# Kernel tuning notes

Hardware: AMD Instinct MI355X
Metric: run time of the kernel (lower is better)

The kernel has to match this reference:

```python
import jax, jax.numpy as jnp
import numpy as np

N_NODES = 100000
NNZ = 3200000
DIM = 256
HOPS = 3


def setup_inputs() -> dict:
    key = jax.random.key(0)
    ks = jax.random.split(key, 8)
    m = jax.random.normal(ks[0], (N_NODES, DIM), dtype=jnp.float32)
    vals = jax.random.uniform(ks[1], (NNZ,), dtype=jnp.float32)
    scale = 1.0 / np.sqrt(DIM)
    Wn = jax.random.normal(ks[2], (HOPS, DIM, DIM), dtype=jnp.float32) * scale
    bn = jax.random.normal(ks[3], (HOPS, DIM), dtype=jnp.float32) * 0.01
    Ws = jax.random.normal(ks[4], (HOPS, DIM, DIM), dtype=jnp.float32) * scale
    bs = jax.random.normal(ks[5], (HOPS, DIM), dtype=jnp.float32) * 0.01
    rows = jax.random.randint(ks[6], (NNZ,), 0, N_NODES, dtype=jnp.int64)
    cols = jax.random.randint(ks[7], (NNZ,), 0, N_NODES, dtype=jnp.int64)
    return {"m": m, "vals": vals, "Wn": Wn, "bn": bn, "Ws": Ws, "bs": bs,
            "rows": rows, "cols": cols}


def reference(m, vals, Wn, bn, Ws, bs, rows, cols):
    # GraphMerge.forward (dropout is identity at eval / rate 0):
    # per hop: H_n = SpMM(A, H) @ Wn^T + bn ; H_s = H @ Ws^T + bs ;
    # H = H_n + H_s ; ELU except after last hop.
    N = m.shape[0]
    hop_num = Wn.shape[0]
    H = m
    for i in range(hop_num):
        # SpMM via edge-list gather + segment_sum (same math as CSR matmul)
        msg = H[cols] * vals[:, None]                     # [nnz, d]
        Hn = jax.ops.segment_sum(msg, rows, num_segments=N)  # [N, d]
        Hn = Hn @ Wn[i].T + bn[i]
        Hs = H @ Ws[i].T + bs[i]
        H = Hn + Hs
        if i != hop_num - 1:
            H = jax.nn.elu(H)
    return H
```

## Files before the change

kernel.cpp:

```cpp
#include <hip/hip_runtime.h>
#include <hip/hip_bf16.h>

typedef unsigned short ushort_t;
using bf16x8 = __attribute__((ext_vector_type(8))) __bf16;
using f32x4  = __attribute__((ext_vector_type(4))) float;

#define NDIM 256

__device__ __forceinline__ float bf2f(ushort_t u) {
    union { unsigned int i; float f; } x; x.i = ((unsigned int)u) << 16; return x.f;
}
__device__ __forceinline__ ushort_t f2bf(float f) {
    unsigned int u = __float_as_uint(f);
    unsigned int r = (u + 0x7FFFu + ((u >> 16) & 1u)) >> 16;
    return (ushort_t)r;
}
__device__ __forceinline__ float ldf(const void* p, int i, int isbf) {
    return isbf ? bf2f(((const ushort_t*)p)[i]) : ((const float*)p)[i];
}
__device__ __forceinline__ int get_idx(const void* arr, int i, int is64) {
    if (is64) return (int)((const long long*)arr)[i];
    return ((const int*)arr)[i];
}

__global__ void k_probe(const unsigned int* __restrict__ w, int* __restrict__ flag) {
    __shared__ int cnt_in;
    if (threadIdx.x == 0) cnt_in = 0;
    __syncthreads();
    int local = 0;
    for (int i = threadIdx.x; i < 4096; i += blockDim.x) {
        unsigned int e = (w[i] >> 7) & 0xFFu;
        if (e >= 110u && e <= 135u) local++;
    }
    atomicAdd(&cnt_in, local);
    __syncthreads();
    if (threadIdx.x == 0) *flag = (cnt_in >= 2048) ? 1 : 0;
}

__global__ void k_detect(const unsigned int* __restrict__ rows_w, int nnz, int* __restrict__ flag) {
    __shared__ int nz;
    if (threadIdx.x == 0) nz = 0;
    __syncthreads();
    int samples = min(nnz / 2, 4096);
    for (int i = threadIdx.x; i < samples; i += blockDim.x) {
        if (rows_w[2 * i + 1] != 0u) atomicAdd(&nz, 1);
    }
    __syncthreads();
    if (threadIdx.x == 0) *flag = (nz == 0) ? 1 : 0;
}

__global__ void k_cvt_m(const void* __restrict__ src, ushort_t* __restrict__ dst, int n,
                        const int* __restrict__ flag) {
    int i = blockIdx.x * blockDim.x + threadIdx.x;
    if (i >= n) return;
    int isbf = *flag;
    dst[i] = isbf ? ((const ushort_t*)src)[i] : f2bf(((const float*)src)[i]);
}

__global__ void k_bias(const void* __restrict__ bn, const void* __restrict__ bs,
                       float* __restrict__ bc, int n, const int* __restrict__ flag) {
    int i = blockIdx.x * blockDim.x + threadIdx.x;
    if (i >= n) return;
    int isbf = *flag;
    bc[i] = ldf(bn, i, isbf) + ldf(bs, i, isbf);
}

__global__ void k_wpack(const void* __restrict__ Wn, const void* __restrict__ Ws,
                        ushort_t* __restrict__ bpack, int total, const int* __restrict__ flag) {
    int t = blockIdx.x * blockDim.x + threadIdx.x;
    if (t >= total) return;
    int isbf  = *flag;
    int j     = t & 7;
    int lane  = (t >> 3) & 63;
    int ntile = (t >> 9) & 15;
    int kstep = (t >> 13) & 15;
    int hop   = t >> 17;
    int k = (kstep << 5) + ((lane >> 4) << 3) + j;
    int n = (ntile << 4) + (lane & 15);
    int kk = k & 255;
    float w = (k < 256) ? ldf(Wn, hop * 65536 + n * 256 + kk, isbf)
                        : ldf(Ws, hop * 65536 + n * 256 + kk, isbf);
    ushort_t hi = f2bf(w);
    float lo = w - bf2f(hi);
    int base = ((((hop << 4) + kstep) << 5) + (ntile << 1)) * 512 + (lane << 3) + j;
    bpack[base]       = hi;
    bpack[base + 512] = f2bf(lo);
}

__global__ void k_hist(const void* __restrict__ rows, int* __restrict__ cnt, int nnz,
                       const int* __restrict__ flag) {
    int is64 = *flag;
    int i = blockIdx.x * blockDim.x + threadIdx.x;
    if (i < nnz) atomicAdd(&cnt[get_idx(rows, i, is64)], 1);
}

__global__ void k_chunksum(const int* __restrict__ cnt, int* __restrict__ csum, int n) {
    __shared__ int s[256];
    int i = blockIdx.x * 256 + threadIdx.x;
    int v = (i < n) ? cnt[i] : 0;
    s[threadIdx.x] = v;
    __syncthreads();
    for (int off = 128; off > 0; off >>= 1) {
        if (threadIdx.x < off) s[threadIdx.x] += s[threadIdx.x + off];
        __syncthreads();
    }
    if (threadIdx.x == 0) csum[blockIdx.x] = s[0];
}

__global__ void k_scanchunks(const int* __restrict__ csum, int* __restrict__ coff, int nchunks) {
    __shared__ int a[512], b[512];
    int t = threadIdx.x;
    int v = (t < nchunks) ? csum[t] : 0;
    a[t] = v;
    __syncthreads();
    int* src = a; int* dst = b;
    for (int off = 1; off < 512; off <<= 1) {
        dst[t] = src[t] + ((t >= off) ? src[t - off] : 0);
        __syncthreads();
        int* tmp = src; src = dst; dst = tmp;
    }
    if (t < nchunks) coff[t] = src[t] - v;
}

__global__ void k_scanwrite(const int* __restrict__ cnt, const int* __restrict__ coff,
                            int* __restrict__ row_start, int* __restrict__ row_cur,
                            int n, int nnz) {
    __shared__ int a[256], b[256];
    int t = threadIdx.x;
    int i = blockIdx.x * 256 + t;
    int v = (i < n) ? cnt[i] : 0;
    a[t] = v;
    __syncthreads();
    int* src = a; int* dst = b;
    for (int off = 1; off < 256; off <<= 1) {
        dst[t] = src[t] + ((t >= off) ? src[t - off] : 0);
        __syncthreads();
        int* tmp = src; src = dst; dst = tmp;
    }
    int excl = src[t] - v + coff[blockIdx.x];
    if (i < n) { row_start[i] = excl; row_cur[i] = excl; }
    if (i == n) row_start[n] = nnz;
}

__global__ void k_scatter(const void* __restrict__ rows, const void* __restrict__ cols,
                          const void* __restrict__ vals, int* __restrict__ row_cur,
                          int2* __restrict__ edata, int nnz,
                          const int* __restrict__ iflag, const int* __restrict__ fflag) {
    int is64 = *iflag;
    int isbf = *fflag;
    int i = blockIdx.x * blockDim.x + threadIdx.x;
    if (i >= nnz) return;
    int r = get_idx(rows, i, is64);
    int c = get_idx(cols, i, is64);
    float v = ldf(vals, i, isbf);
    int p = atomicAdd(&row_cur[r], 1);
    edata[p] = make_int2(c, __float_as_int(v));
}

__global__ void k_spmm(const ushort_t* __restrict__ hb, const int* __restrict__ row_start,
                       const int2* __restrict__ edata, ushort_t* __restrict__ hn, int n) {
    int wid = (blockIdx.x * blockDim.x + threadIdx.x) >> 6;
    if (wid >= n) return;
    wid = __builtin_amdgcn_readfirstlane(wid);
    int lane = threadIdx.x & 63;
    int e0 = row_start[wid];
    int e1 = row_start[wid + 1];
    float a0 = 0.f, a1 = 0.f, a2 = 0.f, a3 = 0.f;
    int off = lane * 4;
    for (int e = e0; e < e1; ++e) {
        int2 ed = edata[e];
        float v = __int_as_float(ed.y);
        ushort4 h = *reinterpret_cast<const ushort4*>(hb + (((long)ed.x) << 8) + off);
        a0 += bf2f(h.x) * v;
        a1 += bf2f(h.y) * v;
        a2 += bf2f(h.z) * v;
        a3 += bf2f(h.w) * v;
    }
    ushort4 o;
    o.x = f2bf(a0); o.y = f2bf(a1); o.z = f2bf(a2); o.w = f2bf(a3);
    *reinterpret_cast<ushort4*>(hn + (((long)wid) << 8) + off) = o;
}

__device__ __forceinline__ void stage32k(const ushort_t* __restrict__ src, ushort_t* dstlds, int tid) {
    const char* s = (const char*)src;
    char* d = (char*)dstlds;
    #pragma unroll
    for (int i = 0; i < 8; ++i) {
        int off = i * 4096 + tid * 16;
        __builtin_amdgcn_global_load_lds(
            (const __attribute__((address_space(1))) unsigned int*)(s + off),
            (__attribute__((address_space(3))) unsigned int*)(d + off),
            16, 0, 0);
    }
}

__global__ __launch_bounds__(256, 2) void k_gemm_mfma(
        const ushort_t* __restrict__ hn, const ushort_t* __restrict__ hb,
        const ushort_t* __restrict__ bpack, const float* __restrict__ bc,
        void* __restrict__ dst, int applyElu, int writeF32, int nvalid) {
    __shared__ __align__(16) ushort_t lds[2][16384];
    int tid  = threadIdx.x;
    int wave = tid >> 6, lane = tid & 63;
    int wm = wave >> 1, wn = wave & 1;
    int rowbase = blockIdx.x * 128 + wm * 64;
    int lr = lane & 15;
    int lk = (lane >> 4) << 3;

    f32x4 acc[4][8];
    #pragma unroll
    for (int mf = 0; mf < 4; ++mf)
        #pragma unroll
        for (int nf = 0; nf < 8; ++nf) acc[mf][nf] = (f32x4){0.f, 0.f, 0.f, 0.f};

    stage32k(bpack, &lds[0][0], tid);
    int cur = 0;
    #pragma unroll 1
    for (int ks = 0; ks < 16; ++ks) {
        const ushort_t* asrc = (ks < 8) ? hn : hb;
        int kcol = ((ks & 7) << 5) + lk;
        bf16x8 af[4];
        #pragma unroll
        for (int mf = 0; mf < 4; ++mf) {
            long row = rowbase + mf * 16 + lr;
            af[mf] = *(const bf16x8*)(asrc + (row << 8) + kcol);
        }
        if (ks < 15) stage32k(bpack + (ks + 1) * 16384, &lds[cur ^ 1][0], tid);
        __syncthreads();
        const ushort_t* bb = &lds[cur][0];
        #pragma unroll
        for (int nf = 0; nf < 8; ++nf) {
            const ushort_t* fp = bb + ((((wn << 3) + nf) << 1) << 9) + (lane << 3);
            bf16x8 bhi = *(const bf16x8*)(fp);
            bf16x8 blo = *(const bf16x8*)(fp + 512);
            #pragma unroll
            for (int mf = 0; mf < 4; ++mf) {
                acc[mf][nf] = __builtin_amdgcn_mfma_f32_16x16x32_bf16(af[mf], bhi, acc[mf][nf], 0, 0, 0);
                acc[mf][nf] = __builtin_amdgcn_mfma_f32_16x16x32_bf16(af[mf], blo, acc[mf][nf], 0, 0, 0);
            }
        }
        __syncthreads();
        cur ^= 1;
    }

    int colb = wn << 7;
    float bcv[8];
    #pragma unroll
    for (int nf = 0; nf < 8; ++nf) bcv[nf] = bc[colb + (nf << 4) + lr];
    int rsub = (lane >> 4) << 2;
    #pragma unroll
    for (int mf = 0; mf < 4; ++mf) {
        #pragma unroll
        for (int r = 0; r < 4; ++r) {
            int row = rowbase + mf * 16 + rsub + r;
            if (row < nvalid) {
                #pragma unroll
                for (int nf = 0; nf < 8; ++nf) {
                    float v = acc[mf][nf][r] + bcv[nf];
                    if (applyElu) v = (v > 0.f) ? v : expm1f(v);
                    int col = colb + (nf << 4) + lr;
                    if (writeF32) ((float*)dst)[(((long)row) << 8) + col] = v;
                    else          ((ushort_t*)dst)[(((long)row) << 8) + col] = f2bf(v);
                }
            }
        }
    }
}

extern "C" void kernel_launch(void* const* d_in, const int* in_sizes, int n_in,
                              void* d_out, int out_size, void* d_ws, size_t ws_size,
                              hipStream_t stream) {
    const void* m    = d_in[0];
    const void* vals = d_in[1];
    const void* Wn   = d_in[2];
    const void* bn   = d_in[3];
    const void* Ws   = d_in[4];
    const void* bs   = d_in[5];
    const void* rows = d_in[6];
    const void* cols = d_in[7];

    const int N    = in_sizes[0] / NDIM;
    const int nnz  = in_sizes[1];
    const int hops = in_sizes[3] / NDIM;
    const size_t mpad = ((size_t)N + 127) & ~(size_t)127;

    char* p = (char*)d_ws;
    ushort_t* Hb    = (ushort_t*)p; p += mpad * NDIM * 2;
    ushort_t* Hn    = (ushort_t*)p; p += mpad * NDIM * 2;
    ushort_t* Bpack = (ushort_t*)p; p += (size_t)hops * 262144 * 2;
    float* Bc       = (float*)p; p += (size_t)hops * 256 * 4;
    int* cnt        = (int*)p; p += ((size_t)N + 256) * 4;
    int* row_start  = (int*)p; p += ((size_t)N + 256) * 4;
    int* row_cur    = (int*)p; p += ((size_t)N + 256) * 4;
    int* csum       = (int*)p; p += 512 * 4;
    int* coff       = (int*)p; p += 512 * 4;
    int* iflag      = (int*)p; p += 64;
    int* fflag      = (int*)p; p += 64;
    p = (char*)(((uintptr_t)p + 15) & ~(uintptr_t)15);
    int2* edata = (int2*)p; p += (size_t)nnz * 8;

    hipMemsetAsync(cnt, 0, (size_t)(N + 1) * sizeof(int), stream);
    if (mpad > (size_t)N) {
        hipMemsetAsync(Hb + (size_t)N * NDIM, 0, (mpad - N) * NDIM * 2, stream);
        hipMemsetAsync(Hn + (size_t)N * NDIM, 0, (mpad - N) * NDIM * 2, stream);
    }

    k_probe<<<1, 256, 0, stream>>>((const unsigned int*)m, fflag);
    k_detect<<<1, 256, 0, stream>>>((const unsigned int*)rows, nnz, iflag);

    int nm = N * NDIM;
    k_cvt_m<<<(nm + 255) / 256, 256, 0, stream>>>(m, Hb, nm, fflag);

    int nb = hops * 256;
    k_bias<<<(nb + 255) / 256, 256, 0, stream>>>(bn, bs, Bc, nb, fflag);

    int wtotal = hops << 17;
    k_wpack<<<(wtotal + 255) / 256, 256, 0, stream>>>(Wn, Ws, Bpack, wtotal, fflag);

    k_hist<<<(nnz + 255) / 256, 256, 0, stream>>>(rows, cnt, nnz, iflag);

    int nchunks = (N + 255) / 256;
    k_chunksum<<<nchunks, 256, 0, stream>>>(cnt, csum, N);
    k_scanchunks<<<1, 512, 0, stream>>>(csum, coff, nchunks);
    k_scanwrite<<<nchunks, 256, 0, stream>>>(cnt, coff, row_start, row_cur, N, nnz);
    k_scatter<<<(nnz + 255) / 256, 256, 0, stream>>>(rows, cols, vals, row_cur, edata, nnz, iflag, fflag);

    int spmm_blocks = (N + 3) / 4;
    int gemm_blocks = (int)(mpad / 128);

    for (int hop = 0; hop < hops; ++hop) {
        k_spmm<<<spmm_blocks, 256, 0, stream>>>(Hb, row_start, edata, Hn, N);
        int last = (hop == hops - 1);
        void* dst = last ? d_out : (void*)Hb;
        k_gemm_mfma<<<gemm_blocks, 256, 0, stream>>>(
            Hn, Hb,
            Bpack + (size_t)hop * 262144,
            Bc + (size_t)hop * 256,
            dst, last ? 0 : 1, last ? 1 : 0, N);
    }
}
```

Measured before the change: 1.586 ms.

## Replace direct CSR scatter with two-pass bucketed binning and XCD-aware placement

```diff
diff --git a/kernel.cpp b/kernel.cpp
--- a/kernel.cpp
+++ b/kernel.cpp
@@ -6,6 +6,8 @@
 using f32x4  = __attribute__((ext_vector_type(4))) float;
 
 #define NDIM 256
+#define BINB 128
+#define PLACE_G 2
 
 __device__ __forceinline__ float bf2f(ushort_t u) {
     union { unsigned int i; float f; } x; x.i = ((unsigned int)u) << 16; return x.f;
@@ -142,19 +144,75 @@
     if (i == n) row_start[n] = nnz;
 }
 
-__global__ void k_scatter(const void* __restrict__ rows, const void* __restrict__ cols,
-                          const void* __restrict__ vals, int* __restrict__ row_cur,
-                          int2* __restrict__ edata, int nnz,
-                          const int* __restrict__ iflag, const int* __restrict__ fflag) {
-    int is64 = *iflag;
-    int isbf = *fflag;
-    int i = blockIdx.x * blockDim.x + threadIdx.x;
-    if (i >= nnz) return;
-    int r = get_idx(rows, i, is64);
-    int c = get_idx(cols, i, is64);
-    float v = ldf(vals, i, isbf);
-    int p = atomicAdd(&row_cur[r], 1);
-    edata[p] = make_int2(c, __float_as_int(v));
+__global__ void k_binit(const int* __restrict__ row_start, int* __restrict__ bucket_cur,
+                        int* __restrict__ bstart, int n, int sh) {
+    int b = threadIdx.x;
+    if (b <= BINB) {
+        int idx = b << sh;
+        if (idx > n) idx = n;
+        int rs = row_start[idx];
+        bstart[b] = rs;
+        if (b < BINB) bucket_cur[b] = rs;
+    }
+}
+
+__global__ __launch_bounds__(256) void k_bin(
+        const void* __restrict__ rows, const void* __restrict__ cols,
+        const void* __restrict__ vals, int* __restrict__ bucket_cur,
+        int4* __restrict__ tmp, int nnz, int sh,
+        const int* __restrict__ iflag, const int* __restrict__ fflag) {
+    __shared__ int cntL[BINB];
+    __shared__ int curL[BINB];
+    int is64 = *iflag, isbf = *fflag;
+    int tid = threadIdx.x;
+    int base = blockIdx.x * 4096;
+    if (tid < BINB) cntL[tid] = 0;
+    __syncthreads();
+    int r[16], b[16];
+    #pragma unroll
+    for (int j = 0; j < 16; ++j) {
+        int idx = base + (j << 8) + tid;
+        if (idx < nnz) {
+            r[j] = get_idx(rows, idx, is64);
+            b[j] = r[j] >> sh;
+            atomicAdd(&cntL[b[j]], 1);
+        } else b[j] = -1;
+    }
+    __syncthreads();
+    if (tid < BINB) curL[tid] = atomicAdd(&bucket_cur[tid], cntL[tid]);
+    __syncthreads();
+    #pragma unroll
+    for (int j = 0; j < 16; ++j) {
+        int idx = base + (j << 8) + tid;
+        if (idx < nnz) {
+            int c = get_idx(cols, idx, is64);
+            float v = ldf(vals, idx, isbf);
+            int p = atomicAdd(&curL[b[j]], 1);
+            tmp[p] = make_int4(r[j], c, __float_as_int(v), 0);
+        }
+    }
+}
+
+__global__ __launch_bounds__(256) void k_place(
+        const int4* __restrict__ tmp, const int* __restrict__ bstart,
+        int* __restrict__ row_cur, int2* __restrict__ edata) {
+    int blk = blockIdx.x;
+    int xcd = blk & 7;
+    int q   = blk >> 3;
+    int g   = q & (PLACE_G - 1);
+    int bq  = q >> 1;
+    int b   = (bq << 3) | xcd;
+    int e0 = bstart[b], e1 = bstart[b + 1];
+    int len = e1 - e0;
+    if (len <= 0) return;
+    int sub = (len + PLACE_G - 1) / PLACE_G;
+    int es = e0 + g * sub;
+    int ee = min(es + sub, e1);
+    for (int e = es + threadIdx.x; e < ee; e += 256) {
+        int4 ed = tmp[e];
+        int p = atomicAdd(&row_cur[ed.x], 1);
+        edata[p] = make_int2(ed.y, ed.z);
+    }
 }
 
 __global__ void k_spmm(const ushort_t* __restrict__ hb, const int* __restrict__ row_start,
@@ -293,15 +351,24 @@
     int* row_cur    = (int*)p; p += ((size_t)N + 256) * 4;
     int* csum       = (int*)p; p += 512 * 4;
     int* coff       = (int*)p; p += 512 * 4;
+    int* bucket_cur = (int*)p; p += 256 * 4;
+    int* bstart     = (int*)p; p += 256 * 4;
     int* iflag      = (int*)p; p += 64;
     int* fflag      = (int*)p; p += 64;
     p = (char*)(((uintptr_t)p + 15) & ~(uintptr_t)15);
     int2* edata = (int2*)p; p += (size_t)nnz * 8;
 
+    int4* tmp;
+    if ((size_t)nnz * 16 <= mpad * NDIM * 2) {
+        tmp = (int4*)Hn;
+    } else {
+        p = (char*)(((uintptr_t)p + 15) & ~(uintptr_t)15);
+        tmp = (int4*)p; p += (size_t)nnz * 16;
+    }
+
     hipMemsetAsync(cnt, 0, (size_t)(N + 1) * sizeof(int), stream);
     if (mpad > (size_t)N) {
         hipMemsetAsync(Hb + (size_t)N * NDIM, 0, (mpad - N) * NDIM * 2, stream);
-        hipMemsetAsync(Hn + (size_t)N * NDIM, 0, (mpad - N) * NDIM * 2, stream);
     }
 
     k_probe<<<1, 256, 0, stream>>>((const unsigned int*)m, fflag);
@@ -322,7 +389,17 @@
     k_chunksum<<<nchunks, 256, 0, stream>>>(cnt, csum, N);
     k_scanchunks<<<1, 512, 0, stream>>>(csum, coff, nchunks);
     k_scanwrite<<<nchunks, 256, 0, stream>>>(cnt, coff, row_start, row_cur, N, nnz);
-    k_scatter<<<(nnz + 255) / 256, 256, 0, stream>>>(rows, cols, vals, row_cur, edata, nnz, iflag, fflag);
+
+    int sh = 0;
+    while (((N - 1) >> sh) >= BINB) sh++;
+
+    k_binit<<<1, 256, 0, stream>>>(row_start, bucket_cur, bstart, N, sh);
+    k_bin<<<(nnz + 4095) / 4096, 256, 0, stream>>>(rows, cols, vals, bucket_cur, tmp, nnz, sh, iflag, fflag);
+    k_place<<<(BINB / 8) * PLACE_G * 8, 256, 0, stream>>>(tmp, bstart, row_cur, edata);
+
+    if (mpad > (size_t)N) {
+        hipMemsetAsync(Hn + (size_t)N * NDIM, 0, (mpad - N) * NDIM * 2, stream);
+    }
 
     int spmm_blocks = (N + 3) / 4;
     int gemm_blocks = (int)(mpad / 128);
```

Result: faster. 1.487 ms (-6.3%).
